# Kernel optimization log

Measured on AMD Instinct MI355X. Metric: run time of the kernel, lower is better.

The kernel has to match this reference:

```python
import jax, jax.numpy as jnp
import numpy as np

ROPE_BASE = 10000.0

def rope_tables(n, r):
    inv = 1.0 / (ROPE_BASE ** (jnp.arange(0, r, 2, dtype=jnp.float32) / r))  # [r/2]
    ang = jnp.arange(n, dtype=jnp.float32)[:, None] * inv[None, :]           # [n, r/2]
    cos = jnp.concatenate([jnp.cos(ang), jnp.cos(ang)], axis=-1)             # [n, r]
    sin = jnp.concatenate([jnp.sin(ang), jnp.sin(ang)], axis=-1)
    return cos, sin

def apply_rope(x, cos, sin):
    # x: [B, H, T, r]; cos/sin: [T, r]
    half = x.shape[-1] // 2
    x_rot = jnp.concatenate([-x[..., half:], x[..., :half]], axis=-1)
    return x * cos + x_rot * sin

def setup_inputs() -> dict:
    key = jax.random.key(0)
    ks = jax.random.split(key, 8)
    B, S, L = 2, 1024, 1024
    dim_q, h, k, d_c, d_cq, r = 2048, 16, 128, 512, 1536, 64
    w = 0.02  # weight scale to keep activations numerically tame
    return {
        'hidden_q': jax.random.normal(ks[0], (B, S, dim_q), jnp.float32),
        'kv_c':     jax.random.normal(ks[1], (B, L, d_c), jnp.float32),
        'Wq':       jax.random.normal(ks[2], (h * k, dim_q), jnp.float32) * w,
        'w_kc_q':   jax.random.normal(ks[3], (h, k, d_cq), jnp.float32) * w,
        'W_qr':     jax.random.normal(ks[4], (h, d_cq, r), jnp.float32) * (w / np.sqrt(r)),
        'W_kr':     jax.random.normal(ks[5], (h, d_c, r), jnp.float32) * w,
        'w_kc_kv':  jax.random.normal(ks[6], (h, k, d_c), jnp.float32) * w,
        'Wo':       jax.random.normal(ks[7], (dim_q, h * k), jnp.float32) * w,
    }

def reference(hidden_q, kv_c, Wq, w_kc_q, W_qr, W_kr, w_kc_kv, Wo):
    B, S, _ = hidden_q.shape
    L = kv_c.shape[1]
    h, k, _ = w_kc_q.shape
    r = W_qr.shape[-1]
    # q projection: [B,S,h,k]
    q_hk = (hidden_q @ Wq.T).reshape(B, S, h, k)
    # low-rank expand to q-compressed space then retrieval space
    q_big = jnp.einsum('bshk,hkq->bshq', q_hk, w_kc_q)          # [B,S,h,d_cq]
    q_r = jnp.einsum('bshq,hqr->bhsr', q_big, W_qr)             # [B,h,S,r]
    k_r = jnp.einsum('bld,hdr->bhlr', kv_c, W_kr)               # [B,h,L,r]
    cos_S, sin_S = rope_tables(S, r)
    cos_L, sin_L = rope_tables(L, r)
    q_r = apply_rope(q_r, cos_S, sin_S)
    k_r = apply_rope(k_r, cos_L, sin_L)
    # attention in retrieval space, values are compressed kv (shared across heads)
    scores = jnp.einsum('bhsr,bhlr->bhsl', q_r, k_r)            # scale baked into W_qr
    attn = jax.nn.softmax(scores, axis=-1)
    ctx_c = jnp.einsum('bhsl,bld->bhsd', attn, kv_c)            # [B,h,S,d_c]
    # decompress per head: w_kc_kv is [h,k,d_c]
    ctx_lat = jnp.einsum('bhsd,hkd->bshk', ctx_c, w_kc_kv).reshape(B, S, h * k)
    return ctx_lat @ Wo.T
```

## Files before the change

### kernel.cpp

```cpp
#include <hip/hip_runtime.h>
#include <math.h>
#include <stdint.h>


typedef __attribute__((ext_vector_type(8))) short short8;
typedef __attribute__((ext_vector_type(4))) float f32x4;

#define GLOAD16(gsrc, ldst)                                                            \
  __builtin_amdgcn_global_load_lds((const __attribute__((address_space(1))) void*)(gsrc), \
                                   (__attribute__((address_space(3))) void*)(ldst), 16, 0, 0)

__device__ inline uint16_t f2b(float x) {
  uint32_t u = __builtin_bit_cast(uint32_t, x);
  u += 0x7fff + ((u >> 16) & 1);
  return (uint16_t)(u >> 16);
}
__device__ inline float b2f(uint16_t b) {
  uint32_t u = ((uint32_t)b) << 16;
  return __builtin_bit_cast(float, u);
}
__device__ inline uint32_t cvtpk_bf16(float lo, float hi) {
  uint32_t d;
  asm("v_cvt_pk_bf16_f32 %0, %1, %2" : "=v"(d) : "v"(lo), "v"(hi));
  return d;
}

__global__ __launch_bounds__(256) void convert5_kernel(
    const float* __restrict__ s0, uint16_t* __restrict__ t0, const float* __restrict__ s1,
    uint16_t* __restrict__ t1, const float* __restrict__ s2, uint16_t* __restrict__ t2,
    const float* __restrict__ s3, uint16_t* __restrict__ t3, const float* __restrict__ s4,
    uint16_t* __restrict__ t4, float* __restrict__ cosK, float* __restrict__ sinK,
    float* __restrict__ cosQ, float* __restrict__ sinQ) {
  int bid = blockIdx.x;
  if (bid >= 6656) {
    const float LOG2E = 1.44269504088896341f;
    int idx = (bid - 6656) * 256 + threadIdx.x;
    int s = idx >> 6, j = idx & 63;
    int i = j & 31;
    float inv = powf(10000.0f, -(float)(2 * i) / 64.0f);
    float ang = (float)s * inv;
    float c = cosf(ang), sn = sinf(ang);
    cosK[idx] = c;
    sinK[idx] = sn;
    cosQ[idx] = c * LOG2E;
    sinQ[idx] = sn * LOG2E;
    return;
  }
  const float* s;
  uint16_t* t;
  int off;
  if (bid < 2048) { s = s0; t = t0; off = bid; }
  else if (bid < 2560) { s = s1; t = t1; off = bid - 2048; }
  else if (bid < 3072) { s = s2; t = t2; off = bid - 2560; }
  else if (bid < 5120) { s = s3; t = t3; off = bid - 3072; }
  else { s = s4; t = t4; off = bid - 5120; }
  int i = off * 256 + threadIdx.x;
  const float4* s4v = (const float4*)s;
  float4 a = s4v[i * 2], b = s4v[i * 2 + 1];
  union {
    uint16_t u[8];
    uint4 v;
  } o;
  o.u[0] = f2b(a.x); o.u[1] = f2b(a.y); o.u[2] = f2b(a.z); o.u[3] = f2b(a.w);
  o.u[4] = f2b(b.x); o.u[5] = f2b(b.y); o.u[6] = f2b(b.z); o.u[7] = f2b(b.w);
  ((uint4*)t)[i] = o.v;
}

__global__ __launch_bounds__(256) void transpose3_kernel(
    const float* __restrict__ Wq, uint16_t* __restrict__ WqT, const float* __restrict__ W_qr,
    uint16_t* __restrict__ WqrT, const float* __restrict__ W_kr, uint16_t* __restrict__ WkrT) {
  __shared__ float t[32][33];
  int bid = blockIdx.x;
  const float* src;
  uint16_t* dst;
  int R, C, r0, c0;
  if (bid < 4096) {
    src = Wq; dst = WqT; R = 2048; C = 2048;
    r0 = (bid & 63) * 32; c0 = (bid >> 6) * 32;
  } else if (bid < 5632) {
    int b = bid - 4096;
    int z = b / 96, rem = b % 96;
    src = W_qr + (size_t)z * 98304; dst = WqrT + (size_t)z * 98304;
    R = 1536; C = 64;
    r0 = (rem >> 1) * 32; c0 = (rem & 1) * 32;
  } else {
    int b = bid - 5632;
    int z = b / 32, rem = b % 32;
    src = W_kr + (size_t)z * 32768; dst = WkrT + (size_t)z * 32768;
    R = 512; C = 64;
    r0 = (rem >> 1) * 32; c0 = (rem & 1) * 32;
  }
  int tr = threadIdx.x >> 5, tc = threadIdx.x & 31;
#pragma unroll
  for (int i = 0; i < 4; ++i) t[tr + i * 8][tc] = src[(size_t)(r0 + tr + i * 8) * C + c0 + tc];
  __syncthreads();
#pragma unroll
  for (int i = 0; i < 4; ++i)
    dst[(size_t)(c0 + tr + i * 8) * R + r0 + tc] = f2b(t[tc][tr + i * 8]);
}

template <int BM, int EPI, int SPLITK = 1>
__global__ __launch_bounds__(256) void gemm_mfma_kernel(const uint16_t* __restrict__ A,
                                                        const uint16_t* __restrict__ Bt,
                                                        void* __restrict__ Cv, int K, int lda,
                                                        int ldb, int ldc, int aZ, int bZ, int cZ,
                                                        const float* __restrict__ rc,
                                                        const float* __restrict__ rs) {
  constexpr int MT = BM / 32;
  __shared__ __align__(16) uint16_t As[2][BM * 64];
  __shared__ __align__(16) uint16_t Bs[2][128 * 64];
  int z = blockIdx.z;
  if (SPLITK > 1) {
    int zh = z / SPLITK, zk = z % SPLITK;
    A += (size_t)zh * aZ + (size_t)zk * K;
    Bt += (size_t)zh * bZ + (size_t)zk * K;
  } else {
    A += (size_t)z * aZ;
    Bt += (size_t)z * bZ;
  }
  int m0 = blockIdx.x * BM, n0 = blockIdx.y * 128;
  int tid = threadIdx.x;
  int wave = tid >> 6, lane = tid & 63;
  int wm = wave >> 1, wn = wave & 1;
  int rS = lane >> 3, sl = lane & 7;
  int lr = lane >> 4, lc = lane & 15;

  auto stage = [&](int k0, int buf) {
#pragma unroll
    for (int i = 0; i < MT; ++i) {
      int idx = wave * MT + i;
      int row = idx * 8 + rS;
      GLOAD16(A + (size_t)(m0 + row) * lda + k0 + ((sl ^ (row & 7)) << 3),
              (uint8_t*)As[buf] + idx * 1024);
    }
#pragma unroll
    for (int i = 0; i < 4; ++i) {
      int idx = wave * 4 + i;
      int row = idx * 8 + rS;
      GLOAD16(Bt + (size_t)(n0 + row) * ldb + k0 + ((sl ^ (row & 7)) << 3),
              (uint8_t*)Bs[buf] + idx * 1024);
    }
  };

  f32x4 acc[MT][4] = {};
  stage(0, 0);
  int cur = 0;
  for (int k0 = 0; k0 < K; k0 += 64) {
    __syncthreads();
    if (k0 + 64 < K) stage(k0 + 64, cur ^ 1);
    short8 af[MT][2], bf[4][2];
#pragma unroll
    for (int t = 0; t < MT; ++t)
#pragma unroll
      for (int ks = 0; ks < 2; ++ks) {
        int slot = ks * 4 + lr;
        int ra = wm * (BM / 2) + t * 16 + lc;
        af[t][ks] =
            *(const short8*)((const uint8_t*)As[cur] + ra * 128 + ((slot ^ (ra & 7)) << 4));
      }
#pragma unroll
    for (int t = 0; t < 4; ++t)
#pragma unroll
      for (int ks = 0; ks < 2; ++ks) {
        int slot = ks * 4 + lr;
        int rb = wn * 64 + t * 16 + lc;
        bf[t][ks] =
            *(const short8*)((const uint8_t*)Bs[cur] + rb * 128 + ((slot ^ (rb & 7)) << 4));
      }
    __builtin_amdgcn_s_setprio(1);
#pragma unroll
    for (int mt = 0; mt < MT; ++mt)
#pragma unroll
      for (int nt = 0; nt < 4; ++nt) {
        acc[mt][nt] =
            __builtin_amdgcn_mfma_f32_16x16x32_bf16(af[mt][0], bf[nt][0], acc[mt][nt], 0, 0, 0);
        acc[mt][nt] =
            __builtin_amdgcn_mfma_f32_16x16x32_bf16(af[mt][1], bf[nt][1], acc[mt][nt], 0, 0, 0);
      }
    __builtin_amdgcn_s_setprio(0);
    cur ^= 1;
  }
  if (EPI == 3) {
#pragma unroll
    for (int mt = 0; mt < MT; ++mt)
#pragma unroll
      for (int nt = 0; nt < 4; ++nt)
#pragma unroll
        for (int r = 0; r < 4; ++r) {
          int m = m0 + wm * (BM / 2) + mt * 16 + lr * 4 + r;
          int n = n0 + wn * 64 + nt * 16 + lc;
          int pos = m & 1023, j = n & 63;
          float x = acc[mt][nt][r];
          float prt = acc[mt][nt ^ 2][r];
          float rot = (nt & 2) ? prt : -prt;
          float v = fmaf(x, rc[pos * 64 + j], rot * rs[pos * 64 + j]);
          ((uint16_t*)Cv)[(size_t)m * ldc + n] = f2b(v);
        }
  } else {
#pragma unroll
    for (int mt = 0; mt < MT; ++mt)
#pragma unroll
      for (int nt = 0; nt < 4; ++nt)
#pragma unroll
        for (int r = 0; r < 4; ++r) {
          int m = m0 + wm * (BM / 2) + mt * 16 + lr * 4 + r;
          int n = n0 + wn * 64 + nt * 16 + lc;
          float v = acc[mt][nt][r];
          if (EPI == 0)
            ((float*)Cv)[(size_t)z * cZ + (size_t)m * ldc + n] = v;
          else if (EPI == 1)
            ((uint16_t*)Cv)[(size_t)z * cZ + (size_t)m * ldc + n] = f2b(v);
          else
            ((uint16_t*)Cv)[((size_t)((m >> 10) * 2048 + n)) * 1024 + (m & 1023)] = f2b(v);
        }
  }
}

__global__ __launch_bounds__(256) void reduce1_kernel(const float* __restrict__ tp,
                                                      uint16_t* __restrict__ tmpT) {
  int gid = blockIdx.x * 256 + threadIdx.x;
  int zh = gid >> 13, e = gid & 8191;
  const float* b = tp + (size_t)zh * 32768 + e;
  tmpT[gid] = f2b(b[0] + b[8192] + b[16384] + b[24576]);
}

__global__ __launch_bounds__(512, 4) void flash3_kernel(const uint16_t* __restrict__ qrb,
                                                        const uint16_t* __restrict__ krb,
                                                        const uint16_t* __restrict__ VhT,
                                                        uint16_t* __restrict__ ctxlatb) {
  __shared__ __align__(16) uint8_t lds[67584];
  int bh = blockIdx.x;
  int b = bh >> 4, h = bh & 15;
  int s0 = blockIdx.y * 64;
  int tid = threadIdx.x, wave = tid >> 6, lane = tid & 63;
  int ig = wave >> 2, w = wave & 3;
  int lr = lane >> 4, lc = lane & 15;
  int rS = lane >> 3, sl = lane & 7;

  uint8_t* Ks = lds + ig * 8192;
  uint8_t* Vs = lds + 16384 + ig * 16384;
  uint8_t* Ps = lds + 49152 + wave * 2304;

  const uint16_t* qrow = qrb + (size_t)(b * 1024 + s0 + w * 16 + lc) * 1024 + h * 64;
  short8 qa[2];
  qa[0] = *(const short8*)(qrow + lr * 8);
  qa[1] = *(const short8*)(qrow + 32 + lr * 8);

  float m_run = -1e30f, l_run = 0.f;
  f32x4 o[8] = {};

  uint8_t* psW = Ps + lc * 144 + lr * 8;
  const uint8_t* psR = Ps + lc * 144 + lr * 16;

  const uint16_t* krbase = krb + (size_t)(b * 1024) * 1024 + h * 64;
  const uint16_t* vtbase = VhT + (size_t)(b * 2048 + h * 128) * 1024;

  auto stageKV = [&](int l0) {
#pragma unroll
    for (int i = 0; i < 2; ++i) {
      int idx = w * 2 + i;
      int row = idx * 8 + rS;
      GLOAD16(krbase + (size_t)(l0 + row) * 1024 + ((sl ^ (row & 7)) << 3), Ks + idx * 1024);
    }
#pragma unroll
    for (int i = 0; i < 4; ++i) {
      int idx = w * 4 + i;
      int row = idx * 8 + rS;
      GLOAD16(vtbase + (size_t)row * 1024 + l0 + ((sl ^ (row & 7)) << 3), Vs + idx * 1024);
    }
  };

  for (int t = 0; t < 8; ++t) {
    int l0 = ig * 512 + t * 64;
    __syncthreads();
    stageKV(l0);
    __syncthreads();

    f32x4 sc[4];
    __builtin_amdgcn_s_setprio(1);
#pragma unroll
    for (int nt = 0; nt < 4; ++nt) {
      int rowk = nt * 16 + lc;
      short8 kb0 = *(const short8*)(Ks + rowk * 128 + ((lr ^ (rowk & 7)) << 4));
      short8 kb1 = *(const short8*)(Ks + rowk * 128 + (((4 + lr) ^ (rowk & 7)) << 4));
      f32x4 z = {};
      z = __builtin_amdgcn_mfma_f32_16x16x32_bf16(kb0, qa[0], z, 0, 0, 0);
      sc[nt] = __builtin_amdgcn_mfma_f32_16x16x32_bf16(kb1, qa[1], z, 0, 0, 0);
    }
    __builtin_amdgcn_s_setprio(0);

    float mx = fmaxf(fmaxf(fmaxf(sc[0][0], sc[0][1]), fmaxf(sc[0][2], sc[0][3])),
                     fmaxf(fmaxf(sc[1][0], sc[1][1]), fmaxf(sc[1][2], sc[1][3])));
    float mx2 = fmaxf(fmaxf(fmaxf(sc[2][0], sc[2][1]), fmaxf(sc[2][2], sc[2][3])),
                      fmaxf(fmaxf(sc[3][0], sc[3][1]), fmaxf(sc[3][2], sc[3][3])));
    mx = fmaxf(mx, mx2);
    mx = fmaxf(mx, __shfl_xor(mx, 16));
    mx = fmaxf(mx, __shfl_xor(mx, 32));

    bool grow = mx > m_run + 8.0f;
    bool upd = (__ballot(grow) != 0ULL);
    float scale;
    if (upd) {
      float mn = fmaxf(m_run, mx);
      scale = exp2f(m_run - mn);
      m_run = mn;
    }

    float ps = 0.f;
#pragma unroll
    for (int nt = 0; nt < 4; ++nt) {
#pragma unroll
      for (int rp = 0; rp < 2; ++rp) {
        float p0 = exp2f(sc[nt][rp * 2] - m_run);
        float p1 = exp2f(sc[nt][rp * 2 + 1] - m_run);
        ps += p0 + p1;
        *(uint32_t*)(psW + nt * 32 + rp * 4) = cvtpk_bf16(p0, p1);
      }
    }
    ps += __shfl_xor(ps, 16);
    ps += __shfl_xor(ps, 32);

    if (upd) {
      l_run = l_run * scale + ps;
      float sc0 = __shfl(scale, lr * 4 + 0);
      float sc1 = __shfl(scale, lr * 4 + 1);
      float sc2 = __shfl(scale, lr * 4 + 2);
      float sc3 = __shfl(scale, lr * 4 + 3);
#pragma unroll
      for (int nt = 0; nt < 8; ++nt) {
        o[nt][0] *= sc0;
        o[nt][1] *= sc1;
        o[nt][2] *= sc2;
        o[nt][3] *= sc3;
      }
    } else {
      l_run += ps;
    }

    short8 pa[2];
    pa[0] = *(const short8*)(psR);
    pa[1] = *(const short8*)(psR + 64);
    __builtin_amdgcn_s_setprio(1);
#pragma unroll
    for (int nt = 0; nt < 8; ++nt) {
      int rowv = nt * 16 + lc;
      short8 vb0 = *(const short8*)(Vs + rowv * 128 + ((lr ^ (rowv & 7)) << 4));
      short8 vb1 = *(const short8*)(Vs + rowv * 128 + (((4 + lr) ^ (rowv & 7)) << 4));
      o[nt] = __builtin_amdgcn_mfma_f32_16x16x32_bf16(pa[0], vb0, o[nt], 0, 0, 0);
      o[nt] = __builtin_amdgcn_mfma_f32_16x16x32_bf16(pa[1], vb1, o[nt], 0, 0, 0);
    }
    __builtin_amdgcn_s_setprio(0);
  }

  __syncthreads();
  float2* mlx = (float2*)(lds + 49152);
  if (lr == 0) mlx[(ig * 4 + w) * 16 + lc] = make_float2(m_run, l_run);
  __syncthreads();
  float2 e0 = mlx[(0 * 4 + w) * 16 + lc];
  float2 e1 = mlx[(1 * 4 + w) * 16 + lc];
  float M = fmaxf(e0.x, e1.x);
  float a0 = exp2f(e0.x - M), a1 = exp2f(e1.x - M);
  float dinv = 1.0f / (e0.y * a0 + e1.y * a1);
  float myA = ig ? a1 : a0;
  float ar[4], dr[4];
#pragma unroll
  for (int r = 0; r < 4; ++r) {
    ar[r] = __shfl(myA, lr * 4 + r);
    dr[r] = __shfl(dinv, lr * 4 + r);
  }
  float* O1 = (float*)lds;
  int qb = w * 16 + lr * 4;
  if (ig == 1) {
#pragma unroll
    for (int nt = 0; nt < 8; ++nt)
#pragma unroll
      for (int r = 0; r < 4; ++r) O1[(qb + r) * 130 + nt * 16 + lc] = o[nt][r] * ar[r];
  }
  __syncthreads();
  if (ig == 0) {
    uint16_t* orow = ctxlatb + (size_t)(b * 1024 + s0 + w * 16) * 2048 + h * 128;
#pragma unroll
    for (int nt = 0; nt < 8; ++nt)
#pragma unroll
      for (int r = 0; r < 4; ++r) {
        float v = (o[nt][r] * ar[r] + O1[(qb + r) * 130 + nt * 16 + lc]) * dr[r];
        orow[(size_t)(lr * 4 + r) * 2048 + nt * 16 + lc] = f2b(v);
      }
  }
}

extern "C" void kernel_launch(void* const* d_in, const int* in_sizes, int n_in,
                              void* d_out, int out_size, void* d_ws, size_t ws_size,
                              hipStream_t stream) {
  const float* hidden_q = (const float*)d_in[0];
  const float* kv_c = (const float*)d_in[1];
  const float* Wq = (const float*)d_in[2];
  const float* w_kc_q = (const float*)d_in[3];
  const float* W_qr = (const float*)d_in[4];
  const float* W_kr = (const float*)d_in[5];
  const float* w_kc_kv = (const float*)d_in[6];
  const float* Wo = (const float*)d_in[7];
  float* out = (float*)d_out;

  const size_t MB = 1024 * 1024;
  uint8_t* base = (uint8_t*)d_ws;
  uint16_t* Wob = (uint16_t*)(base + 0 * MB);
  uint16_t* qrb = (uint16_t*)(base + 8 * MB);
  uint16_t* krb = (uint16_t*)(base + 12 * MB);
  uint16_t* VhT = (uint16_t*)(base + 16 * MB);
  uint16_t* ctxlatb = (uint16_t*)(base + 24 * MB);
  float* cosK = (float*)(base + 32 * MB);
  float* sinK = (float*)(base + 32 * MB + 262144);
  float* cosQ = (float*)(base + 32 * MB + 524288);
  float* sinQ = (float*)(base + 32 * MB + 786432);
  uint16_t* hqb = (uint16_t*)(base + 33 * MB);
  uint16_t* kvb = (uint16_t*)(base + 41 * MB);
  uint16_t* wkvb = (uint16_t*)(base + 43 * MB);
  uint16_t* WqT = (uint16_t*)(base + 45 * MB);
  uint16_t* WqrT = (uint16_t*)(base + 53 * MB);
  uint16_t* wkcqb = (uint16_t*)(base + 56 * MB);
  float* tmp1 = (float*)(base + 62 * MB);
  uint16_t* tmpT = (uint16_t*)(base + 64 * MB);
  uint16_t* WkrT = (uint16_t*)(base + 64 * MB + 262144);

  convert5_kernel<<<dim3(6912), dim3(256), 0, stream>>>(hidden_q, hqb, kv_c, kvb, w_kc_kv, wkvb,
                                                        Wo, Wob, w_kc_q, wkcqb, cosK, sinK, cosQ,
                                                        sinQ);
  transpose3_kernel<<<dim3(6144), dim3(256), 0, stream>>>(Wq, WqT, (const float*)W_qr, WqrT,
                                                          (const float*)W_kr, WkrT);
  gemm_mfma_kernel<64, 0, 4><<<dim3(1, 1, 64), dim3(256), 0, stream>>>(
      WqrT, wkcqb, tmp1, 384, 1536, 1536, 128, 98304, 196608, 8192, nullptr, nullptr);
  reduce1_kernel<<<dim3(512), dim3(256), 0, stream>>>(tmp1, tmpT);
  uint16_t* WfoldT = wkcqb;
  gemm_mfma_kernel<64, 1><<<dim3(1, 16, 16), dim3(256), 0, stream>>>(
      tmpT, WqT, WfoldT, 128, 128, 2048, 2048, 8192, 128, 131072, nullptr, nullptr);
  gemm_mfma_kernel<64, 3><<<dim3(32, 8), dim3(256), 0, stream>>>(hqb, WfoldT, qrb, 2048, 2048,
                                                                 2048, 1024, 0, 0, 0, cosQ, sinQ);
  gemm_mfma_kernel<64, 3><<<dim3(32, 8), dim3(256), 0, stream>>>(kvb, WkrT, krb, 512, 512, 512,
                                                                 1024, 0, 0, 0, cosK, sinK);
  gemm_mfma_kernel<128, 2><<<dim3(16, 16), dim3(256), 0, stream>>>(kvb, wkvb, VhT, 512, 512, 512,
                                                                   0, 0, 0, 0, nullptr, nullptr);
  flash3_kernel<<<dim3(32, 16), dim3(512), 0, stream>>>(qrb, krb, VhT, ctxlatb);
  gemm_mfma_kernel<128, 0><<<dim3(16, 16), dim3(256), 0, stream>>>(ctxlatb, Wob, out, 2048, 2048,
                                                                   2048, 2048, 0, 0, 0, nullptr,
                                                                   nullptr);
}
```

Measured before the change: 154.2 us.

## Double-buffer KV staging in flash kernel and drop split-L merge

The flash attention kernel switches from two wave groups that each handle half of the L range (merged at the end through LDS) to all 8 waves each owning 16 query rows over the full L range. K/V tiles are double-buffered, so the next tile's global-to-LDS loads are issued before computing on the current one, removing one barrier per iteration and the final cross-group softmax merge. The grid halves to 128 query rows per block and launch bounds drop to 2 blocks per CU. The V-projection and output GEMMs also move to 64 tiles with twice as many blocks. The exchange is fewer flash blocks and lower occupancy in return for overlap and simpler epilogue work.

```diff
diff --git a/kernel.cpp b/kernel.cpp
--- a/kernel.cpp
+++ b/kernel.cpp
@@ -224,24 +224,21 @@
   tmpT[gid] = f2b(b[0] + b[8192] + b[16384] + b[24576]);
 }
 
-__global__ __launch_bounds__(512, 4) void flash3_kernel(const uint16_t* __restrict__ qrb,
+__global__ __launch_bounds__(512, 2) void flash3_kernel(const uint16_t* __restrict__ qrb,
                                                         const uint16_t* __restrict__ krb,
                                                         const uint16_t* __restrict__ VhT,
                                                         uint16_t* __restrict__ ctxlatb) {
   __shared__ __align__(16) uint8_t lds[67584];
   int bh = blockIdx.x;
   int b = bh >> 4, h = bh & 15;
-  int s0 = blockIdx.y * 64;
+  int s0 = blockIdx.y * 128;
   int tid = threadIdx.x, wave = tid >> 6, lane = tid & 63;
-  int ig = wave >> 2, w = wave & 3;
   int lr = lane >> 4, lc = lane & 15;
   int rS = lane >> 3, sl = lane & 7;
 
-  uint8_t* Ks = lds + ig * 8192;
-  uint8_t* Vs = lds + 16384 + ig * 16384;
   uint8_t* Ps = lds + 49152 + wave * 2304;
 
-  const uint16_t* qrow = qrb + (size_t)(b * 1024 + s0 + w * 16 + lc) * 1024 + h * 64;
+  const uint16_t* qrow = qrb + (size_t)(b * 1024 + s0 + wave * 16 + lc) * 1024 + h * 64;
   short8 qa[2];
   qa[0] = *(const short8*)(qrow + lr * 8);
   qa[1] = *(const short8*)(qrow + 32 + lr * 8);
@@ -255,26 +252,30 @@
   const uint16_t* krbase = krb + (size_t)(b * 1024) * 1024 + h * 64;
   const uint16_t* vtbase = VhT + (size_t)(b * 2048 + h * 128) * 1024;
 
-  auto stageKV = [&](int l0) {
-#pragma unroll
-    for (int i = 0; i < 2; ++i) {
-      int idx = w * 2 + i;
-      int row = idx * 8 + rS;
-      GLOAD16(krbase + (size_t)(l0 + row) * 1024 + ((sl ^ (row & 7)) << 3), Ks + idx * 1024);
-    }
-#pragma unroll
-    for (int i = 0; i < 4; ++i) {
-      int idx = w * 4 + i;
-      int row = idx * 8 + rS;
-      GLOAD16(vtbase + (size_t)row * 1024 + l0 + ((sl ^ (row & 7)) << 3), Vs + idx * 1024);
+  auto stageKV = [&](int l0, int buf) {
+#pragma unroll
+    for (int i = 0; i < 3; ++i) {
+      int g = wave * 3 + i;
+      if (g < 8) {
+        int row = g * 8 + rS;
+        GLOAD16(krbase + (size_t)(l0 + row) * 1024 + ((sl ^ (row & 7)) << 3),
+                lds + buf * 8192 + g * 1024);
+      } else {
+        int v = g - 8;
+        int row = v * 8 + rS;
+        GLOAD16(vtbase + (size_t)row * 1024 + l0 + ((sl ^ (row & 7)) << 3),
+                lds + 16384 + buf * 16384 + v * 1024);
+      }
     }
   };
 
-  for (int t = 0; t < 8; ++t) {
-    int l0 = ig * 512 + t * 64;
+  stageKV(0, 0);
+  int cur = 0;
+  for (int t = 0; t < 16; ++t) {
     __syncthreads();
-    stageKV(l0);
-    __syncthreads();
+    if (t < 15) stageKV((t + 1) * 64, cur ^ 1);
+    const uint8_t* Ks = lds + cur * 8192;
+    const uint8_t* Vs = lds + 16384 + cur * 16384;
 
     f32x4 sc[4];
     __builtin_amdgcn_s_setprio(1);
@@ -350,43 +351,18 @@
       o[nt] = __builtin_amdgcn_mfma_f32_16x16x32_bf16(pa[1], vb1, o[nt], 0, 0, 0);
     }
     __builtin_amdgcn_s_setprio(0);
-  }
-
-  __syncthreads();
-  float2* mlx = (float2*)(lds + 49152);
-  if (lr == 0) mlx[(ig * 4 + w) * 16 + lc] = make_float2(m_run, l_run);
-  __syncthreads();
-  float2 e0 = mlx[(0 * 4 + w) * 16 + lc];
-  float2 e1 = mlx[(1 * 4 + w) * 16 + lc];
-  float M = fmaxf(e0.x, e1.x);
-  float a0 = exp2f(e0.x - M), a1 = exp2f(e1.x - M);
-  float dinv = 1.0f / (e0.y * a0 + e1.y * a1);
-  float myA = ig ? a1 : a0;
-  float ar[4], dr[4];
-#pragma unroll
-  for (int r = 0; r < 4; ++r) {
-    ar[r] = __shfl(myA, lr * 4 + r);
-    dr[r] = __shfl(dinv, lr * 4 + r);
-  }
-  float* O1 = (float*)lds;
-  int qb = w * 16 + lr * 4;
-  if (ig == 1) {
-#pragma unroll
-    for (int nt = 0; nt < 8; ++nt)
-#pragma unroll
-      for (int r = 0; r < 4; ++r) O1[(qb + r) * 130 + nt * 16 + lc] = o[nt][r] * ar[r];
-  }
-  __syncthreads();
-  if (ig == 0) {
-    uint16_t* orow = ctxlatb + (size_t)(b * 1024 + s0 + w * 16) * 2048 + h * 128;
-#pragma unroll
-    for (int nt = 0; nt < 8; ++nt)
-#pragma unroll
-      for (int r = 0; r < 4; ++r) {
-        float v = (o[nt][r] * ar[r] + O1[(qb + r) * 130 + nt * 16 + lc]) * dr[r];
-        orow[(size_t)(lr * 4 + r) * 2048 + nt * 16 + lc] = f2b(v);
-      }
-  }
+    cur ^= 1;
+  }
+
+  float li[4];
+#pragma unroll
+  for (int r = 0; r < 4; ++r) li[r] = 1.0f / __shfl(l_run, lr * 4 + r);
+  uint16_t* orow = ctxlatb + (size_t)(b * 1024 + s0 + wave * 16) * 2048 + h * 128;
+#pragma unroll
+  for (int nt = 0; nt < 8; ++nt)
+#pragma unroll
+    for (int r = 0; r < 4; ++r)
+      orow[(size_t)(lr * 4 + r) * 2048 + nt * 16 + lc] = f2b(o[nt][r] * li[r]);
 }
 
 extern "C" void kernel_launch(void* const* d_in, const int* in_sizes, int n_in,
@@ -438,10 +414,10 @@
                                                                  2048, 1024, 0, 0, 0, cosQ, sinQ);
   gemm_mfma_kernel<64, 3><<<dim3(32, 8), dim3(256), 0, stream>>>(kvb, WkrT, krb, 512, 512, 512,
                                                                  1024, 0, 0, 0, cosK, sinK);
-  gemm_mfma_kernel<128, 2><<<dim3(16, 16), dim3(256), 0, stream>>>(kvb, wkvb, VhT, 512, 512, 512,
-                                                                   0, 0, 0, 0, nullptr, nullptr);
-  flash3_kernel<<<dim3(32, 16), dim3(512), 0, stream>>>(qrb, krb, VhT, ctxlatb);
-  gemm_mfma_kernel<128, 0><<<dim3(16, 16), dim3(256), 0, stream>>>(ctxlatb, Wob, out, 2048, 2048,
-                                                                   2048, 2048, 0, 0, 0, nullptr,
-                                                                   nullptr);
-}
+  gemm_mfma_kernel<64, 2><<<dim3(32, 16), dim3(256), 0, stream>>>(kvb, wkvb, VhT, 512, 512, 512, 0,
+                                                                  0, 0, 0, nullptr, nullptr);
+  flash3_kernel<<<dim3(32, 8), dim3(512), 0, stream>>>(qrb, krb, VhT, ctxlatb);
+  gemm_mfma_kernel<64, 0><<<dim3(32, 16), dim3(256), 0, stream>>>(ctxlatb, Wob, out, 2048, 2048,
+                                                                  2048, 2048, 0, 0, 0, nullptr,
+                                                                  nullptr);
+}
```

Measured after the change: 147.5 us. 1.05x faster.
